# Kernel optimization log

Hardware: AMD Instinct MI355X
Metric: run time of the kernel (lower is better)

## Reference

```python
import math
import jax, jax.numpy as jnp
import numpy as np

BS, T, D_MODEL, H = 4, 1024, 1024, 16
D_K = D_MODEL // H


def setup_inputs() -> dict:
    key = jax.random.key(0)
    ks = jax.random.split(key, 16)
    s = 0.02  # weight init scale
    return {
        "q": jax.random.normal(ks[0], (BS, T, D_MODEL), jnp.float32),
        "k": jax.random.normal(ks[1], (BS, T, D_MODEL), jnp.float32),
        "v": jax.random.normal(ks[2], (BS, T, D_MODEL), jnp.float32),
        "pos_emb": jax.random.normal(ks[3], (1, T, D_MODEL), jnp.float32),
        "mask": jnp.ones((BS, T, T), jnp.int32),
        "Wq": jax.random.normal(ks[4], (D_MODEL, D_MODEL), jnp.float32) * s,
        "bq": jax.random.normal(ks[5], (D_MODEL,), jnp.float32) * s,
        "Wk": jax.random.normal(ks[6], (D_MODEL, D_MODEL), jnp.float32) * s,
        "bk": jax.random.normal(ks[7], (D_MODEL,), jnp.float32) * s,
        "Wv": jax.random.normal(ks[8], (D_MODEL, D_MODEL), jnp.float32) * s,
        "bv": jax.random.normal(ks[9], (D_MODEL,), jnp.float32) * s,
        "Wp": jax.random.normal(ks[10], (D_MODEL, D_MODEL), jnp.float32) * s,
        "pos_bias_u": jax.random.normal(ks[11], (H, D_K), jnp.float32) * s,
        "pos_bias_v": jax.random.normal(ks[12], (H, D_K), jnp.float32) * s,
        "Wo": jax.random.normal(ks[13], (D_MODEL, D_MODEL), jnp.float32) * s,
        "bo": jax.random.normal(ks[14], (D_MODEL,), jnp.float32) * s,
    }


def rel_shift(x):
    # x: [b, h, T, P]; Transformer-XL relative shift via pad+reshape
    b, h, t, p = x.shape
    x = jnp.pad(x, ((0, 0), (0, 0), (0, 0), (1, 0)))  # [b,h,T,P+1]
    x = x.reshape(b, h, p + 1, t)[:, :, 1:, :]
    return x.reshape(b, h, t, p)


def reference(q, k, v, pos_emb, mask, Wq, bq, Wk, bk, Wv, bv, Wp,
              pos_bias_u, pos_bias_v, Wo, bo):
    bs, t, d_model = q.shape
    h, d_k = pos_bias_u.shape
    # projections (torch Linear: x @ W.T + b)
    qh = (q @ Wq.T + bq).reshape(bs, t, h, d_k)                      # [b,t,h,d]
    kh = (k @ Wk.T + bk).reshape(bs, t, h, d_k).transpose(0, 2, 1, 3)  # [b,h,s,d]
    vh = (v @ Wv.T + bv).reshape(bs, t, h, d_k).transpose(0, 2, 1, 3)  # [b,h,s,d]
    p = (pos_emb @ Wp.T).reshape(pos_emb.shape[0], -1, h, d_k).transpose(0, 2, 1, 3)  # [1,h,P,d]
    q_u = (qh + pos_bias_u).transpose(0, 2, 1, 3)  # [b,h,t,d]
    q_v = (qh + pos_bias_v).transpose(0, 2, 1, 3)  # [b,h,t,d]
    matrix_ac = jnp.einsum('bhtd,bhsd->bhts', q_u, kh)
    matrix_bd = jnp.einsum('bhtd,hpd->bhtp', q_v, p[0])
    matrix_bd = rel_shift(matrix_bd)
    scores = (matrix_ac + matrix_bd) / math.sqrt(d_k)
    m = mask[:, None, :, :]  # broadcast over heads
    attn = jax.nn.softmax(jnp.where(m == 0, jnp.float32(-10000.0), scores), axis=-1)
    out_h = jnp.einsum('bhts,bhsd->bhtd', attn, vh)
    concat = out_h.transpose(0, 2, 1, 3).reshape(bs, t, d_model)
    output = concat @ Wo.T + bo
    return (output, attn)
```

## Files before the change

### kernel.cpp

```cpp
#include <hip/hip_runtime.h>

typedef _Float16 f16;
typedef __attribute__((ext_vector_type(8))) _Float16 f16x8;
typedef __attribute__((ext_vector_type(4))) float f32x4;

#define LDK 40


__device__ __forceinline__ void stage_f16g(const f16* __restrict__ src, int ld, f16* dst) {
    int t = threadIdx.x;
    int row = t >> 2;
    int c0 = (t & 3) * 8;
    *(f16x8*)(dst + row * LDK + c0) = *(const f16x8*)(src + (size_t)row * ld + c0);
}

__device__ __forceinline__ void stage_vT(const f16* __restrict__ src, f16* dst) {
    int t = threadIdx.x;
    int s = t >> 3;
    int d0 = (t & 7) * 8;
    f16x8 h = *(const f16x8*)(src + (size_t)s * 64 + d0);
#pragma unroll
    for (int j = 0; j < 8; ++j) dst[(d0 + j) * LDK + s] = h[j];
}


__device__ __forceinline__ void mma_step(const f16* As, const f16* Bs, int m_off, int n_off,
                                         f32x4 acc[2][2]) {
    int lane = threadIdx.x & 63;
    int r = lane & 15;
    int kq = (lane >> 4) * 8;
    f16x8 a0 = *(const f16x8*)(As + (m_off + r) * LDK + kq);
    f16x8 a1 = *(const f16x8*)(As + (m_off + 16 + r) * LDK + kq);
    f16x8 b0 = *(const f16x8*)(Bs + (n_off + r) * LDK + kq);
    f16x8 b1 = *(const f16x8*)(Bs + (n_off + 16 + r) * LDK + kq);
    acc[0][0] = __builtin_amdgcn_mfma_f32_16x16x32_f16(a0, b0, acc[0][0], 0, 0, 0);
    acc[0][1] = __builtin_amdgcn_mfma_f32_16x16x32_f16(a0, b1, acc[0][1], 0, 0, 0);
    acc[1][0] = __builtin_amdgcn_mfma_f32_16x16x32_f16(a1, b0, acc[1][0], 0, 0, 0);
    acc[1][1] = __builtin_amdgcn_mfma_f32_16x16x32_f16(a1, b1, acc[1][1], 0, 0, 0);
}

#define GEMM_PROLOGUE()                                         \
    __shared__ f16 As[64 * LDK];                                \
    __shared__ f16 Bs[64 * LDK];                                \
    const int w = threadIdx.x >> 6;                             \
    const int m_off = (w & 1) * 32, n_off = (w >> 1) * 32;      \
    const int lane = threadIdx.x & 63;                          \
    f32x4 zero = {0.f, 0.f, 0.f, 0.f};                          \
    f32x4 acc[2][2] = {{zero, zero}, {zero, zero}};

__global__ __launch_bounds__(256) void cvt_all(
    const float* __restrict__ q, const float* __restrict__ k, const float* __restrict__ v,
    const float* __restrict__ pe, const float* __restrict__ Wq, const float* __restrict__ Wk,
    const float* __restrict__ Wv, const float* __restrict__ Wp, const float* __restrict__ Wo,
    f16* __restrict__ dst) {
    const int seg = blockIdx.y;
    const float* srcs[9] = {q, k, v, pe, Wq, Wk, Wv, Wp, Wo};
    const int sz = (seg < 3) ? 4194304 : 1048576;
    const size_t off = (seg < 3) ? (size_t)seg * 4194304
                                 : (size_t)12582912 + (size_t)(seg - 3) * 1048576;
    const size_t i0 = ((size_t)blockIdx.x * 256 + threadIdx.x) * 16;
    if (i0 >= (size_t)sz) return;
    const float* s = srcs[seg] + i0;
    f16* d = dst + off + i0;
#pragma unroll
    for (int half = 0; half < 2; ++half) {
        float4 u = *(const float4*)(s + half * 8);
        float4 w = *(const float4*)(s + half * 8 + 4);
        f16x8 h;
        h[0] = (f16)u.x; h[1] = (f16)u.y; h[2] = (f16)u.z; h[3] = (f16)u.w;
        h[4] = (f16)w.x; h[5] = (f16)w.y; h[6] = (f16)w.z; h[7] = (f16)w.w;
        *(f16x8*)(d + half * 8) = h;
    }
}

__global__ __launch_bounds__(256) void proj_qkv(
    const f16* __restrict__ qf, const f16* __restrict__ kf, const f16* __restrict__ vf,
    const f16* __restrict__ Wqf, const f16* __restrict__ Wkf, const f16* __restrict__ Wvf,
    const float* __restrict__ bq, const float* __restrict__ bk, const float* __restrict__ bv,
    const float* __restrict__ pbu, const float* __restrict__ pbv,
    f16* __restrict__ q_u, f16* __restrict__ q_v, f16* __restrict__ kh,
    f16* __restrict__ vh) {
    GEMM_PROLOGUE();
    const int z = blockIdx.z;
    const f16* A = (z == 0) ? qf : (z == 1) ? kf : vf;
    const f16* W = (z == 0) ? Wqf : (z == 1) ? Wkf : Wvf;
    const float* bias = (z == 0) ? bq : (z == 1) ? bk : bv;
    const int m0 = blockIdx.y * 64, n0 = blockIdx.x * 64;
    for (int k0 = 0; k0 < 1024; k0 += 32) {
        stage_f16g(A + (size_t)m0 * 1024 + k0, 1024, As);
        stage_f16g(W + (size_t)n0 * 1024 + k0, 1024, Bs);
        __syncthreads();
        mma_step(As, Bs, m_off, n_off, acc);
        __syncthreads();
    }
#pragma unroll
    for (int mt = 0; mt < 2; ++mt)
#pragma unroll
        for (int nt = 0; nt < 2; ++nt)
#pragma unroll
            for (int rr = 0; rr < 4; ++rr) {
                int m = m0 + m_off + mt * 16 + (lane >> 4) * 4 + rr;
                int n = n0 + n_off + nt * 16 + (lane & 15);
                float base = acc[mt][nt][rr] + bias[n];
                int b = m >> 10, t = m & 1023, h = n >> 6, d = n & 63;
                size_t idx = ((size_t)((b * 16 + h) * 1024 + t)) * 64 + d;
                if (z == 0) {
                    q_u[idx] = (f16)(base + pbu[n]);
                    q_v[idx] = (f16)(base + pbv[n]);
                } else if (z == 1) {
                    kh[idx] = (f16)base;
                } else {
                    vh[idx] = (f16)base;
                }
            }
}

__global__ __launch_bounds__(256) void proj_p(const f16* __restrict__ A,
                                              const f16* __restrict__ W,
                                              f16* __restrict__ o1) {
    GEMM_PROLOGUE();
    const int m0 = blockIdx.y * 64;
    const int n0 = blockIdx.x * 64;
    for (int k0 = 0; k0 < 1024; k0 += 32) {
        stage_f16g(A + (size_t)m0 * 1024 + k0, 1024, As);
        stage_f16g(W + (size_t)n0 * 1024 + k0, 1024, Bs);
        __syncthreads();
        mma_step(As, Bs, m_off, n_off, acc);
        __syncthreads();
    }
#pragma unroll
    for (int mt = 0; mt < 2; ++mt)
#pragma unroll
        for (int nt = 0; nt < 2; ++nt)
#pragma unroll
            for (int rr = 0; rr < 4; ++rr) {
                int m = m0 + m_off + mt * 16 + (lane >> 4) * 4 + rr;
                int n = n0 + n_off + nt * 16 + (lane & 15);
                int h = n >> 6, d = n & 63;
                o1[((size_t)h * 1024 + m) * 64 + d] = (f16)acc[mt][nt][rr];
            }
}

__global__ __launch_bounds__(256) void bd_gemm(const f16* __restrict__ qv,
                                               const f16* __restrict__ p,
                                               f16* __restrict__ bds) {
    GEMM_PROLOGUE();
    const int bh = blockIdx.z;
    const int h = bh & 15;
    const int m0 = blockIdx.y * 64, n0 = blockIdx.x * 64;
    const f16* Ab = qv + (size_t)bh * 65536;
    const f16* Bb = p + (size_t)h * 65536;
    for (int k0 = 0; k0 < 64; k0 += 32) {
        stage_f16g(Ab + (size_t)m0 * 64 + k0, 64, As);
        stage_f16g(Bb + (size_t)n0 * 64 + k0, 64, Bs);
        __syncthreads();
        mma_step(As, Bs, m_off, n_off, acc);
        __syncthreads();
    }
    f16* B0 = bds + (size_t)bh * 1048576;
#pragma unroll
    for (int mt = 0; mt < 2; ++mt)
#pragma unroll
        for (int nt = 0; nt < 2; ++nt)
#pragma unroll
            for (int rr = 0; rr < 4; ++rr) {
                int r = m0 + m_off + mt * 16 + (lane >> 4) * 4 + rr;
                int c = n0 + n_off + nt * 16 + (lane & 15);
                float vv = acc[mt][nt][rr];
                if (c >= 1023 - r) {
                    B0[(size_t)r * 1024 + (c + r - 1023)] = (f16)vv;
                } else if (r >= 1) {
                    B0[(size_t)(r - 1) * 1024 + (c + r + 1)] = (f16)vv;
                }
            }
}

__global__ __launch_bounds__(256) void ac_gemm(const f16* __restrict__ qu,
                                               const f16* __restrict__ kh,
                                               f16* __restrict__ bds) {
    GEMM_PROLOGUE();
    const int bh = blockIdx.z;
    const int m0 = blockIdx.y * 64, n0 = blockIdx.x * 64;
    const f16* Ab = qu + (size_t)bh * 65536;
    const f16* Bb = kh + (size_t)bh * 65536;
    for (int k0 = 0; k0 < 64; k0 += 32) {
        stage_f16g(Ab + (size_t)m0 * 64 + k0, 64, As);
        stage_f16g(Bb + (size_t)n0 * 64 + k0, 64, Bs);
        __syncthreads();
        mma_step(As, Bs, m_off, n_off, acc);
        __syncthreads();
    }
#pragma unroll
    for (int mt = 0; mt < 2; ++mt)
#pragma unroll
        for (int nt = 0; nt < 2; ++nt)
#pragma unroll
            for (int rr = 0; rr < 4; ++rr) {
                int i = m0 + m_off + mt * 16 + (lane >> 4) * 4 + rr;
                int j = n0 + n_off + nt * 16 + (lane & 15);
                size_t idx = (size_t)bh * 1048576 + (size_t)i * 1024 + j;
                float bdv = (j == i + 1) ? 0.f : (float)bds[idx];
                bds[idx] = (f16)((acc[mt][nt][rr] + bdv) * 0.125f);
            }
}

__global__ __launch_bounds__(256) void softmax_pv(const f16* __restrict__ scores,
                                                  const int* __restrict__ mask,
                                                  const f16* __restrict__ vh,
                                                  float* __restrict__ attn,
                                                  f16* __restrict__ oh) {
    const int bh = blockIdx.y;
    const int i0 = blockIdx.x * 64;
    const int b = bh >> 4, h = bh & 15;
    const f16* S = scores + (size_t)bh * 1048576 + (size_t)i0 * 1024;
    const int* MK = mask + ((size_t)b * 1024 + i0) * 1024;
    __shared__ float s_max[64], s_invl[64];

    const int w = threadIdx.x >> 6;
    const int lane = threadIdx.x & 63;

    for (int rr = 0; rr < 16; ++rr) {
        int r = w * 16 + rr;
        const f16* srow = S + (size_t)r * 1024 + lane * 16;
        const int* mrow = MK + (size_t)r * 1024 + lane * 16;
        f16x8 a0 = *(const f16x8*)srow;
        f16x8 a1 = *(const f16x8*)(srow + 8);
        int4 m0 = *(const int4*)mrow;
        int4 m1 = *(const int4*)(mrow + 4);
        int4 m2 = *(const int4*)(mrow + 8);
        int4 m3 = *(const int4*)(mrow + 12);
        int mks[16] = {m0.x, m0.y, m0.z, m0.w, m1.x, m1.y, m1.z, m1.w,
                       m2.x, m2.y, m2.z, m2.w, m3.x, m3.y, m3.z, m3.w};
        float vals[16];
        float mx = -1e30f;
#pragma unroll
        for (int j = 0; j < 16; ++j) {
            float v = (j < 8) ? (float)a0[j] : (float)a1[j - 8];
            if (mks[j] == 0) v = -10000.0f;
            vals[j] = v;
            mx = fmaxf(mx, v);
        }
#pragma unroll
        for (int off = 32; off > 0; off >>= 1) mx = fmaxf(mx, __shfl_xor(mx, off));
        float sum = 0.f;
#pragma unroll
        for (int j = 0; j < 16; ++j) sum += __expf(vals[j] - mx);
#pragma unroll
        for (int off = 32; off > 0; off >>= 1) sum += __shfl_xor(sum, off);
        if (lane == 0) {
            s_max[r] = mx;
            s_invl[r] = 1.f / sum;
        }
    }
    __syncthreads();

    __shared__ f16 As[64 * LDK];
    __shared__ f16 Bs[64 * LDK];
    const int m_off = (w & 1) * 32, n_off = (w >> 1) * 32;
    f32x4 zero = {0.f, 0.f, 0.f, 0.f};
    f32x4 acc[2][2] = {{zero, zero}, {zero, zero}};
    const int r2 = threadIdx.x >> 2;
    const int c2 = (threadIdx.x & 3) * 8;
    const f16* Vb = vh + (size_t)bh * 65536;
    float* arow = attn + (size_t)bh * 1048576 + (size_t)(i0 + r2) * 1024 + c2;

    for (int j0 = 0; j0 < 1024; j0 += 32) {
        f16x8 sv = *(const f16x8*)(S + (size_t)r2 * 1024 + j0 + c2);
        const int* mp = MK + (size_t)r2 * 1024 + j0 + c2;
        int4 mk0 = *(const int4*)mp;
        int4 mk1 = *(const int4*)(mp + 4);
        int mks[8] = {mk0.x, mk0.y, mk0.z, mk0.w, mk1.x, mk1.y, mk1.z, mk1.w};
        float mx = s_max[r2], il = s_invl[r2];
        f16x8 pv;
        float po[8];
#pragma unroll
        for (int j = 0; j < 8; ++j) {
            float s = (float)sv[j];
            if (mks[j] == 0) s = -10000.0f;
            float p = __expf(s - mx) * il;
            po[j] = p;
            pv[j] = (f16)p;
        }
        *(float4*)(arow + j0) = {po[0], po[1], po[2], po[3]};
        *(float4*)(arow + j0 + 4) = {po[4], po[5], po[6], po[7]};
        *(f16x8*)(As + r2 * LDK + c2) = pv;
        stage_vT(Vb + (size_t)j0 * 64, Bs);
        __syncthreads();
        mma_step(As, Bs, m_off, n_off, acc);
        __syncthreads();
    }

#pragma unroll
    for (int mt = 0; mt < 2; ++mt)
#pragma unroll
        for (int nt = 0; nt < 2; ++nt)
#pragma unroll
            for (int rr = 0; rr < 4; ++rr) {
                int t = i0 + m_off + mt * 16 + (lane >> 4) * 4 + rr;
                int d = n_off + nt * 16 + (lane & 15);
                oh[((size_t)(b * 1024 + t)) * 1024 + h * 64 + d] =
                    (f16)acc[mt][nt][rr];
            }
}

__global__ __launch_bounds__(256) void out_gemm(const f16* __restrict__ A,
                                                const f16* __restrict__ W,
                                                const float* __restrict__ bias,
                                                float* __restrict__ out) {
    GEMM_PROLOGUE();
    const int m0 = blockIdx.y * 64;
    const int n0 = blockIdx.x * 64;
    for (int k0 = 0; k0 < 1024; k0 += 32) {
        stage_f16g(A + (size_t)m0 * 1024 + k0, 1024, As);
        stage_f16g(W + (size_t)n0 * 1024 + k0, 1024, Bs);
        __syncthreads();
        mma_step(As, Bs, m_off, n_off, acc);
        __syncthreads();
    }
#pragma unroll
    for (int mt = 0; mt < 2; ++mt)
#pragma unroll
        for (int nt = 0; nt < 2; ++nt)
#pragma unroll
            for (int rr = 0; rr < 4; ++rr) {
                int m = m0 + m_off + mt * 16 + (lane >> 4) * 4 + rr;
                int n = n0 + n_off + nt * 16 + (lane & 15);
                out[(size_t)m * 1024 + n] = acc[mt][nt][rr] + bias[n];
            }
}

extern "C" void kernel_launch(void* const* d_in, const int* in_sizes, int n_in,
                              void* d_out, int out_size, void* d_ws, size_t ws_size,
                              hipStream_t stream) {
    (void)in_sizes; (void)n_in; (void)out_size; (void)ws_size;
    const float* q   = (const float*)d_in[0];
    const float* k   = (const float*)d_in[1];
    const float* v   = (const float*)d_in[2];
    const float* pe  = (const float*)d_in[3];
    const int*   msk = (const int*)d_in[4];
    const float* Wq  = (const float*)d_in[5];
    const float* bq  = (const float*)d_in[6];
    const float* Wk  = (const float*)d_in[7];
    const float* bk  = (const float*)d_in[8];
    const float* Wv  = (const float*)d_in[9];
    const float* bv  = (const float*)d_in[10];
    const float* Wp  = (const float*)d_in[11];
    const float* pbu = (const float*)d_in[12];
    const float* pbv = (const float*)d_in[13];
    const float* Wo  = (const float*)d_in[14];
    const float* bo  = (const float*)d_in[15];

    char* ws = (char*)d_ws;
    f16* cvt = (f16*)(ws + 0);
    f16* qf  = cvt;
    f16* kf  = cvt + 4194304;
    f16* vf  = cvt + 8388608;
    f16* pef = cvt + 12582912;
    f16* Wqf = cvt + 13631488;
    f16* Wkf = cvt + 14680064;
    f16* Wvf = cvt + 15728640;
    f16* Wpf = cvt + 16777216;
    f16* Wof = cvt + 17825792;

    f16* q_u = (f16*)(ws + 37748736);
    f16* q_v = (f16*)(ws + 46137344);
    f16* kh  = (f16*)(ws + 54525952);
    f16* vh  = (f16*)(ws + 62914560);
    f16* pp  = (f16*)(ws + 71303168);
    f16* bds = (f16*)(ws + 73400320);
    f16* oh  = (f16*)(ws + 207618048);

    float* out  = (float*)d_out;
    float* attn = out + 4194304;

    dim3 blk(256);
    cvt_all<<<dim3(1024, 9), blk, 0, stream>>>(q, k, v, pe, Wq, Wk, Wv, Wp, Wo, cvt);
    proj_qkv<<<dim3(16, 64, 3), blk, 0, stream>>>(qf, kf, vf, Wqf, Wkf, Wvf, bq, bk, bv,
                                                  pbu, pbv, q_u, q_v, kh, vh);
    proj_p<<<dim3(16, 16), blk, 0, stream>>>(pef, Wpf, pp);
    bd_gemm<<<dim3(16, 16, 64), blk, 0, stream>>>(q_v, pp, bds);
    ac_gemm<<<dim3(16, 16, 64), blk, 0, stream>>>(q_u, kh, bds);
    softmax_pv<<<dim3(16, 64), blk, 0, stream>>>(bds, msk, vh, attn, oh);
    out_gemm<<<dim3(16, 64), blk, 0, stream>>>(oh, Wof, bo, out);
}
```

Baseline: 703.9 us.

## Fuse BD/AC score GEMMs, rel-shift, softmax and PV into one attention kernel

Replaces the three kernels bd_gemm, ac_gemm and softmax_pv with one fused_attn kernel. It keeps a 64x1024 fp16 score tile in LDS, computes the BD scores, applies the relative shift in shared memory (with an extra row computed for the cross-tile dependency), adds the AC scores, then runs softmax and the PV MFMA. This removes the round trips of the large fp16 score buffer through global memory and two kernel launches. The cost is about 130KB of LDS per block, which limits occupancy to one block per CU, plus extra syncthreads in the shift loop and a scalar dot product for the boundary row.

```diff
diff --git a/kernel.cpp b/kernel.cpp
--- a/kernel.cpp
+++ b/kernel.cpp
@@ -5,7 +5,8 @@
 typedef __attribute__((ext_vector_type(4))) float f32x4;
 
 #define LDK 40
-
+#define SST 1032
+#define BST 72
 
 __device__ __forceinline__ void stage_f16g(const f16* __restrict__ src, int ld, f16* dst) {
     int t = threadIdx.x;
@@ -13,16 +14,6 @@
     int c0 = (t & 3) * 8;
     *(f16x8*)(dst + row * LDK + c0) = *(const f16x8*)(src + (size_t)row * ld + c0);
 }
-
-__device__ __forceinline__ void stage_vT(const f16* __restrict__ src, f16* dst) {
-    int t = threadIdx.x;
-    int s = t >> 3;
-    int d0 = (t & 7) * 8;
-    f16x8 h = *(const f16x8*)(src + (size_t)s * 64 + d0);
-#pragma unroll
-    for (int j = 0; j < 8; ++j) dst[(d0 + j) * LDK + s] = h[j];
-}
-
 
 __device__ __forceinline__ void mma_step(const f16* As, const f16* Bs, int m_off, int n_off,
                                          f32x4 acc[2][2]) {
@@ -40,8 +31,8 @@
 }
 
 #define GEMM_PROLOGUE()                                         \
-    __shared__ f16 As[64 * LDK];                                \
-    __shared__ f16 Bs[64 * LDK];                                \
+    __shared__ __align__(16) f16 As[64 * LDK];                  \
+    __shared__ __align__(16) f16 Bs[64 * LDK];                  \
     const int w = threadIdx.x >> 6;                             \
     const int m_off = (w & 1) * 32, n_off = (w >> 1) * 32;      \
     const int lane = threadIdx.x & 63;                          \
@@ -141,96 +132,163 @@
             }
 }
 
-__global__ __launch_bounds__(256) void bd_gemm(const f16* __restrict__ qv,
-                                               const f16* __restrict__ p,
-                                               f16* __restrict__ bds) {
-    GEMM_PROLOGUE();
-    const int bh = blockIdx.z;
-    const int h = bh & 15;
-    const int m0 = blockIdx.y * 64, n0 = blockIdx.x * 64;
-    const f16* Ab = qv + (size_t)bh * 65536;
-    const f16* Bb = p + (size_t)h * 65536;
-    for (int k0 = 0; k0 < 64; k0 += 32) {
-        stage_f16g(Ab + (size_t)m0 * 64 + k0, 64, As);
-        stage_f16g(Bb + (size_t)n0 * 64 + k0, 64, Bs);
-        __syncthreads();
-        mma_step(As, Bs, m_off, n_off, acc);
-        __syncthreads();
-    }
-    f16* B0 = bds + (size_t)bh * 1048576;
+__global__ __launch_bounds__(256) void fused_attn(
+    const f16* __restrict__ q_u, const f16* __restrict__ q_v,
+    const f16* __restrict__ kh, const f16* __restrict__ pp,
+    const f16* __restrict__ vh, const int* __restrict__ mask,
+    float* __restrict__ attn, f16* __restrict__ oh) {
+    __shared__ __align__(16) f16 Ssc[64 * SST];
+    __shared__ __align__(16) f16 Bt[64 * BST];
+    __shared__ __align__(16) f16 rawX[1024];
+    __shared__ __align__(16) f16 qxrow[64];
+
+    const int bh = blockIdx.y;
+    const int b = bh >> 4, h = bh & 15;
+    const int i0 = blockIdx.x * 64;
+    const int tid = threadIdx.x;
+    const int w = tid >> 6;
+    const int lane = tid & 63;
+    const int m_off = (w & 1) * 32, n_off = (w >> 1) * 32;
+    const int fr = lane & 15;
+    const int kq = (lane >> 4) * 8;
+    const f32x4 zero = {0.f, 0.f, 0.f, 0.f};
+
+    const f16* Qu = q_u + (size_t)bh * 65536;
+    const f16* Qv = q_v + (size_t)bh * 65536;
+    const f16* Kh = kh + (size_t)bh * 65536;
+    const f16* Pp = pp + (size_t)h * 65536;
+    const f16* Vh = vh + (size_t)bh * 65536;
+
+    f16x8 qu_f[2][2], qv_f[2][2];
 #pragma unroll
     for (int mt = 0; mt < 2; ++mt)
 #pragma unroll
-        for (int nt = 0; nt < 2; ++nt)
-#pragma unroll
-            for (int rr = 0; rr < 4; ++rr) {
-                int r = m0 + m_off + mt * 16 + (lane >> 4) * 4 + rr;
-                int c = n0 + n_off + nt * 16 + (lane & 15);
-                float vv = acc[mt][nt][rr];
-                if (c >= 1023 - r) {
-                    B0[(size_t)r * 1024 + (c + r - 1023)] = (f16)vv;
-                } else if (r >= 1) {
-                    B0[(size_t)(r - 1) * 1024 + (c + r + 1)] = (f16)vv;
+        for (int ks = 0; ks < 2; ++ks) {
+            size_t off = (size_t)(i0 + m_off + mt * 16 + fr) * 64 + ks * 32 + kq;
+            qu_f[mt][ks] = *(const f16x8*)(Qu + off);
+            qv_f[mt][ks] = *(const f16x8*)(Qv + off);
+        }
+
+    if (i0 + 64 < 1024 && tid < 8)
+        *(f16x8*)(qxrow + tid * 8) = *(const f16x8*)(Qv + (size_t)(i0 + 64) * 64 + tid * 8);
+
+    for (int j0 = 0; j0 < 1024; j0 += 64) {
+        {
+            int rrow = tid >> 2, c0 = (tid & 3) * 16;
+            const f16* s = Pp + (size_t)(j0 + rrow) * 64 + c0;
+            *(f16x8*)(Bt + rrow * BST + c0) = *(const f16x8*)(s);
+            *(f16x8*)(Bt + rrow * BST + c0 + 8) = *(const f16x8*)(s + 8);
+        }
+        __syncthreads();
+        f32x4 acc[2][2] = {{zero, zero}, {zero, zero}};
+#pragma unroll
+        for (int ks = 0; ks < 2; ++ks) {
+            f16x8 b0 = *(const f16x8*)(Bt + (n_off + fr) * BST + ks * 32 + kq);
+            f16x8 b1 = *(const f16x8*)(Bt + (n_off + 16 + fr) * BST + ks * 32 + kq);
+            acc[0][0] = __builtin_amdgcn_mfma_f32_16x16x32_f16(qv_f[0][ks], b0, acc[0][0], 0, 0, 0);
+            acc[0][1] = __builtin_amdgcn_mfma_f32_16x16x32_f16(qv_f[0][ks], b1, acc[0][1], 0, 0, 0);
+            acc[1][0] = __builtin_amdgcn_mfma_f32_16x16x32_f16(qv_f[1][ks], b0, acc[1][0], 0, 0, 0);
+            acc[1][1] = __builtin_amdgcn_mfma_f32_16x16x32_f16(qv_f[1][ks], b1, acc[1][1], 0, 0, 0);
+        }
+#pragma unroll
+        for (int mt = 0; mt < 2; ++mt)
+#pragma unroll
+            for (int nt = 0; nt < 2; ++nt)
+#pragma unroll
+                for (int rr = 0; rr < 4; ++rr) {
+                    int m = m_off + mt * 16 + (lane >> 4) * 4 + rr;
+                    int c = j0 + n_off + nt * 16 + fr;
+                    Ssc[m * SST + c] = (f16)acc[mt][nt][rr];
                 }
-            }
-}
-
-__global__ __launch_bounds__(256) void ac_gemm(const f16* __restrict__ qu,
-                                               const f16* __restrict__ kh,
-                                               f16* __restrict__ bds) {
-    GEMM_PROLOGUE();
-    const int bh = blockIdx.z;
-    const int m0 = blockIdx.y * 64, n0 = blockIdx.x * 64;
-    const f16* Ab = qu + (size_t)bh * 65536;
-    const f16* Bb = kh + (size_t)bh * 65536;
-    for (int k0 = 0; k0 < 64; k0 += 32) {
-        stage_f16g(Ab + (size_t)m0 * 64 + k0, 64, As);
-        stage_f16g(Bb + (size_t)n0 * 64 + k0, 64, Bs);
-        __syncthreads();
-        mma_step(As, Bs, m_off, n_off, acc);
-        __syncthreads();
-    }
-#pragma unroll
-    for (int mt = 0; mt < 2; ++mt)
-#pragma unroll
-        for (int nt = 0; nt < 2; ++nt)
-#pragma unroll
-            for (int rr = 0; rr < 4; ++rr) {
-                int i = m0 + m_off + mt * 16 + (lane >> 4) * 4 + rr;
-                int j = n0 + n_off + nt * 16 + (lane & 15);
-                size_t idx = (size_t)bh * 1048576 + (size_t)i * 1024 + j;
-                float bdv = (j == i + 1) ? 0.f : (float)bds[idx];
-                bds[idx] = (f16)((acc[mt][nt][rr] + bdv) * 0.125f);
-            }
-}
-
-__global__ __launch_bounds__(256) void softmax_pv(const f16* __restrict__ scores,
-                                                  const int* __restrict__ mask,
-                                                  const f16* __restrict__ vh,
-                                                  float* __restrict__ attn,
-                                                  f16* __restrict__ oh) {
-    const int bh = blockIdx.y;
-    const int i0 = blockIdx.x * 64;
-    const int b = bh >> 4, h = bh & 15;
-    const f16* S = scores + (size_t)bh * 1048576 + (size_t)i0 * 1024;
+        __syncthreads();
+    }
+
+    if (i0 + 64 < 1024) {
+        int p = tid * 4;
+#pragma unroll
+        for (int pi = 0; pi < 4; ++pi) {
+            const f16* pr = Pp + (size_t)(p + pi) * 64;
+            float sacc = 0.f;
+#pragma unroll
+            for (int c = 0; c < 64; c += 8) {
+                f16x8 pv = *(const f16x8*)(pr + c);
+                f16x8 qv8 = *(const f16x8*)(qxrow + c);
+#pragma unroll
+                for (int j = 0; j < 8; ++j) sacc += (float)pv[j] * (float)qv8[j];
+            }
+            rawX[p + pi] = (f16)sacc;
+        }
+    }
+
+    for (int cc = 0; cc < 16; ++cc) {
+        int lr = cc * 4 + w;
+        int r = i0 + lr;
+        int s0 = lane * 16;
+        f16 tmp[16];
+#pragma unroll
+        for (int j = 0; j < 16; ++j) {
+            int s = s0 + j;
+            f16 val;
+            if (s <= r) val = Ssc[lr * SST + (s + 1023 - r)];
+            else if (s == r + 1) val = (f16)0.f;
+            else val = (lr == 63) ? rawX[s - r - 2] : Ssc[(lr + 1) * SST + (s - r - 2)];
+            tmp[j] = val;
+        }
+        __syncthreads();
+        f16x8 o0, o1;
+#pragma unroll
+        for (int j = 0; j < 8; ++j) { o0[j] = tmp[j]; o1[j] = tmp[8 + j]; }
+        *(f16x8*)(Ssc + lr * SST + s0) = o0;
+        *(f16x8*)(Ssc + lr * SST + s0 + 8) = o1;
+        __syncthreads();
+    }
+
+    for (int j0 = 0; j0 < 1024; j0 += 64) {
+        {
+            int rrow = tid >> 2, c0 = (tid & 3) * 16;
+            const f16* s = Kh + (size_t)(j0 + rrow) * 64 + c0;
+            *(f16x8*)(Bt + rrow * BST + c0) = *(const f16x8*)(s);
+            *(f16x8*)(Bt + rrow * BST + c0 + 8) = *(const f16x8*)(s + 8);
+        }
+        __syncthreads();
+        f32x4 acc[2][2] = {{zero, zero}, {zero, zero}};
+#pragma unroll
+        for (int ks = 0; ks < 2; ++ks) {
+            f16x8 b0 = *(const f16x8*)(Bt + (n_off + fr) * BST + ks * 32 + kq);
+            f16x8 b1 = *(const f16x8*)(Bt + (n_off + 16 + fr) * BST + ks * 32 + kq);
+            acc[0][0] = __builtin_amdgcn_mfma_f32_16x16x32_f16(qu_f[0][ks], b0, acc[0][0], 0, 0, 0);
+            acc[0][1] = __builtin_amdgcn_mfma_f32_16x16x32_f16(qu_f[0][ks], b1, acc[0][1], 0, 0, 0);
+            acc[1][0] = __builtin_amdgcn_mfma_f32_16x16x32_f16(qu_f[1][ks], b0, acc[1][0], 0, 0, 0);
+            acc[1][1] = __builtin_amdgcn_mfma_f32_16x16x32_f16(qu_f[1][ks], b1, acc[1][1], 0, 0, 0);
+        }
+#pragma unroll
+        for (int mt = 0; mt < 2; ++mt)
+#pragma unroll
+            for (int nt = 0; nt < 2; ++nt)
+#pragma unroll
+                for (int rr = 0; rr < 4; ++rr) {
+                    int m = m_off + mt * 16 + (lane >> 4) * 4 + rr;
+                    int c = j0 + n_off + nt * 16 + fr;
+                    float sc = ((float)Ssc[m * SST + c] + acc[mt][nt][rr]) * 0.125f;
+                    Ssc[m * SST + c] = (f16)sc;
+                }
+        __syncthreads();
+    }
+
+    float* Ab = attn + (size_t)bh * 1048576;
     const int* MK = mask + ((size_t)b * 1024 + i0) * 1024;
-    __shared__ float s_max[64], s_invl[64];
-
-    const int w = threadIdx.x >> 6;
-    const int lane = threadIdx.x & 63;
-
     for (int rr = 0; rr < 16; ++rr) {
-        int r = w * 16 + rr;
-        const f16* srow = S + (size_t)r * 1024 + lane * 16;
-        const int* mrow = MK + (size_t)r * 1024 + lane * 16;
-        f16x8 a0 = *(const f16x8*)srow;
-        f16x8 a1 = *(const f16x8*)(srow + 8);
-        int4 m0 = *(const int4*)mrow;
-        int4 m1 = *(const int4*)(mrow + 4);
-        int4 m2 = *(const int4*)(mrow + 8);
-        int4 m3 = *(const int4*)(mrow + 12);
-        int mks[16] = {m0.x, m0.y, m0.z, m0.w, m1.x, m1.y, m1.z, m1.w,
-                       m2.x, m2.y, m2.z, m2.w, m3.x, m3.y, m3.z, m3.w};
+        int lr = w * 16 + rr;
+        int c0 = lane * 16;
+        f16x8 a0 = *(const f16x8*)(Ssc + lr * SST + c0);
+        f16x8 a1 = *(const f16x8*)(Ssc + lr * SST + c0 + 8);
+        const int* mrow = MK + (size_t)lr * 1024 + c0;
+        int4 mk0 = *(const int4*)mrow;
+        int4 mk1 = *(const int4*)(mrow + 4);
+        int4 mk2 = *(const int4*)(mrow + 8);
+        int4 mk3 = *(const int4*)(mrow + 12);
+        int mks[16] = {mk0.x, mk0.y, mk0.z, mk0.w, mk1.x, mk1.y, mk1.z, mk1.w,
+                       mk2.x, mk2.y, mk2.z, mk2.w, mk3.x, mk3.y, mk3.z, mk3.w};
         float vals[16];
         float mx = -1e30f;
 #pragma unroll
@@ -244,52 +302,57 @@
         for (int off = 32; off > 0; off >>= 1) mx = fmaxf(mx, __shfl_xor(mx, off));
         float sum = 0.f;
 #pragma unroll
-        for (int j = 0; j < 16; ++j) sum += __expf(vals[j] - mx);
+        for (int j = 0; j < 16; ++j) { vals[j] = __expf(vals[j] - mx); sum += vals[j]; }
 #pragma unroll
         for (int off = 32; off > 0; off >>= 1) sum += __shfl_xor(sum, off);
-        if (lane == 0) {
-            s_max[r] = mx;
-            s_invl[r] = 1.f / sum;
-        }
+        float il = 1.f / sum;
+        float* arow = Ab + (size_t)(i0 + lr) * 1024 + c0;
+        float4 f0 = {vals[0] * il, vals[1] * il, vals[2] * il, vals[3] * il};
+        float4 f1 = {vals[4] * il, vals[5] * il, vals[6] * il, vals[7] * il};
+        float4 f2 = {vals[8] * il, vals[9] * il, vals[10] * il, vals[11] * il};
+        float4 f3 = {vals[12] * il, vals[13] * il, vals[14] * il, vals[15] * il};
+        *(float4*)(arow) = f0;
+        *(float4*)(arow + 4) = f1;
+        *(float4*)(arow + 8) = f2;
+        *(float4*)(arow + 12) = f3;
+        f16x8 p0, p1;
+#pragma unroll
+        for (int j = 0; j < 8; ++j) {
+            p0[j] = (f16)(vals[j] * il);
+            p1[j] = (f16)(vals[8 + j] * il);
+        }
+        *(f16x8*)(Ssc + lr * SST + c0) = p0;
+        *(f16x8*)(Ssc + lr * SST + c0 + 8) = p1;
     }
     __syncthreads();
 
-    __shared__ f16 As[64 * LDK];
-    __shared__ f16 Bs[64 * LDK];
-    const int m_off = (w & 1) * 32, n_off = (w >> 1) * 32;
-    f32x4 zero = {0.f, 0.f, 0.f, 0.f};
     f32x4 acc[2][2] = {{zero, zero}, {zero, zero}};
-    const int r2 = threadIdx.x >> 2;
-    const int c2 = (threadIdx.x & 3) * 8;
-    const f16* Vb = vh + (size_t)bh * 65536;
-    float* arow = attn + (size_t)bh * 1048576 + (size_t)(i0 + r2) * 1024 + c2;
-
-    for (int j0 = 0; j0 < 1024; j0 += 32) {
-        f16x8 sv = *(const f16x8*)(S + (size_t)r2 * 1024 + j0 + c2);
-        const int* mp = MK + (size_t)r2 * 1024 + j0 + c2;
-        int4 mk0 = *(const int4*)mp;
-        int4 mk1 = *(const int4*)(mp + 4);
-        int mks[8] = {mk0.x, mk0.y, mk0.z, mk0.w, mk1.x, mk1.y, mk1.z, mk1.w};
-        float mx = s_max[r2], il = s_invl[r2];
-        f16x8 pv;
-        float po[8];
-#pragma unroll
-        for (int j = 0; j < 8; ++j) {
-            float s = (float)sv[j];
-            if (mks[j] == 0) s = -10000.0f;
-            float p = __expf(s - mx) * il;
-            po[j] = p;
-            pv[j] = (f16)p;
-        }
-        *(float4*)(arow + j0) = {po[0], po[1], po[2], po[3]};
-        *(float4*)(arow + j0 + 4) = {po[4], po[5], po[6], po[7]};
-        *(f16x8*)(As + r2 * LDK + c2) = pv;
-        stage_vT(Vb + (size_t)j0 * 64, Bs);
-        __syncthreads();
-        mma_step(As, Bs, m_off, n_off, acc);
-        __syncthreads();
-    }
-
+    for (int j0 = 0; j0 < 1024; j0 += 64) {
+        {
+            int srow = tid >> 2, d0 = (tid & 3) * 16;
+            const f16* s = Vh + (size_t)(j0 + srow) * 64 + d0;
+            f16x8 h0 = *(const f16x8*)(s);
+            f16x8 h1 = *(const f16x8*)(s + 8);
+#pragma unroll
+            for (int j = 0; j < 8; ++j) {
+                Bt[(d0 + j) * BST + srow] = h0[j];
+                Bt[(d0 + 8 + j) * BST + srow] = h1[j];
+            }
+        }
+        __syncthreads();
+#pragma unroll
+        for (int ks = 0; ks < 2; ++ks) {
+            f16x8 a0 = *(const f16x8*)(Ssc + (m_off + fr) * SST + j0 + ks * 32 + kq);
+            f16x8 a1 = *(const f16x8*)(Ssc + (m_off + 16 + fr) * SST + j0 + ks * 32 + kq);
+            f16x8 b0 = *(const f16x8*)(Bt + (n_off + fr) * BST + ks * 32 + kq);
+            f16x8 b1 = *(const f16x8*)(Bt + (n_off + 16 + fr) * BST + ks * 32 + kq);
+            acc[0][0] = __builtin_amdgcn_mfma_f32_16x16x32_f16(a0, b0, acc[0][0], 0, 0, 0);
+            acc[0][1] = __builtin_amdgcn_mfma_f32_16x16x32_f16(a0, b1, acc[0][1], 0, 0, 0);
+            acc[1][0] = __builtin_amdgcn_mfma_f32_16x16x32_f16(a1, b0, acc[1][0], 0, 0, 0);
+            acc[1][1] = __builtin_amdgcn_mfma_f32_16x16x32_f16(a1, b1, acc[1][1], 0, 0, 0);
+        }
+        __syncthreads();
+    }
 #pragma unroll
     for (int mt = 0; mt < 2; ++mt)
 #pragma unroll
@@ -297,9 +360,8 @@
 #pragma unroll
             for (int rr = 0; rr < 4; ++rr) {
                 int t = i0 + m_off + mt * 16 + (lane >> 4) * 4 + rr;
-                int d = n_off + nt * 16 + (lane & 15);
-                oh[((size_t)(b * 1024 + t)) * 1024 + h * 64 + d] =
-                    (f16)acc[mt][nt][rr];
+                int d = n_off + nt * 16 + fr;
+                oh[((size_t)(b * 1024 + t)) * 1024 + h * 64 + d] = (f16)acc[mt][nt][rr];
             }
 }
 
@@ -367,8 +429,7 @@
     f16* kh  = (f16*)(ws + 54525952);
     f16* vh  = (f16*)(ws + 62914560);
     f16* pp  = (f16*)(ws + 71303168);
-    f16* bds = (f16*)(ws + 73400320);
-    f16* oh  = (f16*)(ws + 207618048);
+    f16* oh  = (f16*)(ws + 73400320);
 
     float* out  = (float*)d_out;
     float* attn = out + 4194304;
@@ -378,8 +439,6 @@
     proj_qkv<<<dim3(16, 64, 3), blk, 0, stream>>>(qf, kf, vf, Wqf, Wkf, Wvf, bq, bk, bv,
                                                   pbu, pbv, q_u, q_v, kh, vh);
     proj_p<<<dim3(16, 16), blk, 0, stream>>>(pef, Wpf, pp);
-    bd_gemm<<<dim3(16, 16, 64), blk, 0, stream>>>(q_v, pp, bds);
-    ac_gemm<<<dim3(16, 16, 64), blk, 0, stream>>>(q_u, kh, bds);
-    softmax_pv<<<dim3(16, 64), blk, 0, stream>>>(bds, msk, vh, attn, oh);
+    fused_attn<<<dim3(16, 64), blk, 0, stream>>>(q_u, q_v, kh, pp, vh, msk, attn, oh);
     out_gemm<<<dim3(16, 64), blk, 0, stream>>>(oh, Wof, bo, out);
 }
```

Result: slower. 776.9 us (+10.4%).
